# Optimization experiments

Hardware: AMD Instinct MI355X
Metric: run time of the kernel (lower is better)

Reference implementation:

```python
import jax, jax.numpy as jnp
import numpy as np
from jax import lax

NQ = 5  # qubits
NL = 3  # circuit layers


def conv2d(x, w, b):
    y = lax.conv_general_dilated(x, w, (1, 1), 'SAME',
                                 dimension_numbers=('NCHW', 'OIHW', 'NCHW'))
    return y + b[None, :, None, None]


def batchnorm(x, g, b, eps=1e-5):
    # training-mode batch statistics over (N,H,W), matching nn.BatchNorm2d in train()
    mu = x.mean((0, 2, 3), keepdims=True)
    var = x.var((0, 2, 3), keepdims=True)
    return g[None, :, None, None] * (x - mu) * lax.rsqrt(var + eps) + b[None, :, None, None]


def maxpool2(x):
    return lax.reduce_window(x, -jnp.inf, lax.max, (1, 1, 2, 2), (1, 1, 2, 2), 'VALID')


def _apply_1q(state, U, w):
    # state: (2,)*NQ, wire w is axis w (PennyLane default.qubit ordering)
    s = jnp.tensordot(U, state, axes=([1], [w]))
    return jnp.moveaxis(s, 0, w)


def _cnot(state, c, t):
    s0 = jnp.take(state, 0, axis=c)
    s1 = jnp.take(state, 1, axis=c)
    ta = t if t < c else t - 1
    s1 = jnp.flip(s1, axis=ta)  # X on target when control=1
    return jnp.stack([s0, s1], axis=c)


def _rx(t):
    c, s = jnp.cos(t / 2), jnp.sin(t / 2)
    return jnp.array([[c, -1j * s], [-1j * s, c]], dtype=jnp.complex64)


def _ry(t):
    c, s = jnp.cos(t / 2), jnp.sin(t / 2)
    return jnp.array([[c, -s], [s, c]], dtype=jnp.complex64)


def _rz(t):
    e = jnp.exp(-1j * t / 2)
    z = jnp.zeros((), jnp.complex64)
    return jnp.array([[e, z], [z, jnp.conj(e)]], dtype=jnp.complex64)


def quantum_circuit(inputs, weights):
    # inputs: (5,), weights: (30,)  -> scalar <Z0 Z1 Z2>
    state = jnp.zeros((2,) * NQ, jnp.complex64).at[(0,) * NQ].set(1.0)
    npl = NQ * 2  # weights per layer = 10
    nw = weights.shape[0]
    for l in range(NL):
        for i in range(NQ):
            state = _apply_1q(state, _rx(inputs[i]), i)
        for i in range(NQ):
            state = _apply_1q(state, _ry(weights[(l * npl + i) % nw]), i)
            state = _apply_1q(state, _rz(weights[(l * npl + i + NQ) % nw]), i)
        for i in range(NQ - 1):
            state = _cnot(state, i, i + 1)
        state = _cnot(state, NQ - 1, 0)
    probs = jnp.abs(state) ** 2
    z = jnp.array([1.0, -1.0], jnp.float32)
    sign = z[:, None, None] * z[None, :, None] * z[None, None, :]  # Z on wires 0,1,2
    return jnp.sum(probs * sign[:, :, :, None, None])


def setup_inputs() -> dict:
    key = jax.random.key(0)
    ks = jax.random.split(key, 12)
    d = {}
    d['x'] = jax.random.normal(ks[0], (256, 1, 224, 224), jnp.float32)
    d['conv1_w'] = jax.random.normal(ks[1], (16, 1, 3, 3), jnp.float32) * 0.1
    d['conv1_b'] = jnp.zeros((16,), jnp.float32)
    d['bn1_g'] = jnp.ones((16,), jnp.float32)
    d['bn1_b'] = jnp.zeros((16,), jnp.float32)
    d['conv2_w'] = jax.random.normal(ks[2], (32, 16, 3, 3), jnp.float32) * 0.05
    d['conv2_b'] = jnp.zeros((32,), jnp.float32)
    d['bn2_g'] = jnp.ones((32,), jnp.float32)
    d['bn2_b'] = jnp.zeros((32,), jnp.float32)
    d['conv3_w'] = jax.random.normal(ks[3], (64, 32, 3, 3), jnp.float32) * 0.05
    d['conv3_b'] = jnp.zeros((64,), jnp.float32)
    d['bn3_g'] = jnp.ones((64,), jnp.float32)
    d['bn3_b'] = jnp.zeros((64,), jnp.float32)
    d['fc1_w'] = jax.random.normal(ks[4], (64, 5), jnp.float32) * 0.1   # (in,out)
    d['fc1_b'] = jnp.zeros((5,), jnp.float32)
    d['ln_g'] = jnp.ones((5,), jnp.float32)
    d['ln_b'] = jnp.zeros((5,), jnp.float32)
    d['q_params'] = jax.random.uniform(ks[5], (30,), jnp.float32)
    d['fc2_w'] = jax.random.normal(ks[6], (1, 32), jnp.float32) * 0.5
    d['fc2_b'] = jnp.zeros((32,), jnp.float32)
    d['fc3_w'] = jax.random.normal(ks[7], (32, 2), jnp.float32) * 0.2
    d['fc3_b'] = jnp.zeros((2,), jnp.float32)
    return d


def reference(x, conv1_w, conv1_b, bn1_g, bn1_b, conv2_w, conv2_b, bn2_g, bn2_b,
              conv3_w, conv3_b, bn3_g, bn3_b, fc1_w, fc1_b, ln_g, ln_b,
              q_params, fc2_w, fc2_b, fc3_w, fc3_b):
    h = maxpool2(jax.nn.relu(batchnorm(conv2d(x, conv1_w, conv1_b), bn1_g, bn1_b)))
    h = maxpool2(jax.nn.relu(batchnorm(conv2d(h, conv2_w, conv2_b), bn2_g, bn2_b)))
    h = maxpool2(jax.nn.relu(batchnorm(conv2d(h, conv3_w, conv3_b), bn3_g, bn3_b)))
    # dropout is identity in eval; adaptive avg pool (1,1) + flatten
    h = h.mean((2, 3))                    # (B, 64)
    h = h @ fc1_w + fc1_b                 # (B, 5)
    mu = h.mean(-1, keepdims=True)
    var = h.var(-1, keepdims=True)
    h = ln_g * (h - mu) * lax.rsqrt(var + 1e-5) + ln_b
    q = jax.vmap(lambda inp: quantum_circuit(inp, q_params))(h)  # (B,)
    q = q[:, None].astype(jnp.float32)    # (B, 1)
    h2 = jax.nn.relu(q @ fc2_w + fc2_b)   # (B, 32)
    logits = h2 @ fc3_w + fc3_b           # (B, 2)
    return jax.nn.log_softmax(logits, axis=1)
```

## Files before the change

kernel.cpp:

```cpp
#include <hip/hip_runtime.h>
#include <hip/hip_bf16.h>


typedef _Float16 f16;
typedef _Float16 f16x2 __attribute__((ext_vector_type(2)));
typedef _Float16 f16x4 __attribute__((ext_vector_type(4)));
typedef _Float16 f16x8 __attribute__((ext_vector_type(8)));
typedef float f32x4 __attribute__((ext_vector_type(4)));
typedef float f32x16 __attribute__((ext_vector_type(16)));

#define DEV static __device__ __forceinline__

DEV float wave_sum(float v) {
#pragma unroll
  for (int off = 32; off > 0; off >>= 1) v += __shfl_xor(v, off, 64);
  return v;
}

__global__ __launch_bounds__(256) void repack(const float* __restrict__ w2,
                                              const float* __restrict__ w3,
                                              f16* __restrict__ Bt2,
                                              f16* __restrict__ Bt3) {
  int t = blockIdx.x * 256 + threadIdx.x;
  int T = gridDim.x * 256;
  for (int i = t; i < 32 * 168; i += T) {
    int oc = i / 168, kk = i - oc * 168;
    float v = 0.f;
    if (kk < 144) {
      int tap = kk >> 4, ic = kk & 15;
      v = w2[(oc * 16 + ic) * 9 + tap];
    }
    Bt2[i] = (f16)v;
  }
  for (int i = t; i < 64 * 296; i += T) {
    int oc = i / 296, kk = i - oc * 296;
    float v = 0.f;
    if (kk < 288) {
      int tap = kk / 32, ic = kk & 31;
      v = w3[(oc * 32 + ic) * 9 + tap];
    }
    Bt3[i] = (f16)v;
  }
}

__global__ __launch_bounds__(64) void finalize(const float* __restrict__ banks,
                                               const float* __restrict__ g,
                                               const float* __restrict__ b,
                                               float* __restrict__ scsh, int C,
                                               float inv_n) {
  int c = blockIdx.x, bk = threadIdx.x;
  float s = banks[bk * 2 * C + c];
  float qq = banks[bk * 2 * C + C + c];
  s = wave_sum(s);
  qq = wave_sum(qq);
  if (bk == 0) {
    float mean = s * inv_n;
    float var = qq * inv_n - mean * mean;
    float sc = g[c] * rsqrtf(var + 1e-5f);
    scsh[c] = sc;
    scsh[C + c] = b[c] - mean * sc;
  }
}

__global__ __launch_bounds__(256) void l1_mfma32(const float* __restrict__ x,
                                                 const float* __restrict__ w1,
                                                 float* __restrict__ banks,
                                                 f16* __restrict__ h1raw) {
  __shared__ f16 xA[18 * 240];
  __shared__ f16 xB[18 * 240];
  __shared__ f16 lrow[4 * 3616];
  __shared__ float lstat[32];
  int bid = blockIdx.x;
  int n = bid / 14, band = bid - n * 14;
  int y0 = band * 16;
  int t = threadIdx.x;
  if (t < 32) lstat[t] = 0.f;
  for (int i = t; i < 1008; i += 256) {
    int r = i / 56, k = i - r * 56;
    int y = y0 - 1 + r;
    float4 v = make_float4(0.f, 0.f, 0.f, 0.f);
    if ((unsigned)y < 224u)
      v = *(const float4*)(x + ((size_t)(n * 224 + y)) * 224 + k * 4);
    f16 h0 = (f16)v.x, h1 = (f16)v.y, h2 = (f16)v.z, h3 = (f16)v.w;
    f16* pa = xA + r * 240 + 4 * k + 1;
    pa[0] = h0; pa[1] = h1; pa[2] = h2; pa[3] = h3;
    f16x4 pk = {h0, h1, h2, h3};
    *(f16x4*)(xB + r * 240 + 4 * k) = pk;
  }
  if (t < 18) {
    xA[t * 240 + 0] = (f16)0.f;
    xA[t * 240 + 225] = (f16)0.f;
    xA[t * 240 + 226] = (f16)0.f;
    xB[t * 240 + 224] = (f16)0.f;
    xB[t * 240 + 225] = (f16)0.f;
  }
  __syncthreads();

  int wave = t >> 6, lane = t & 63;
  int g = lane >> 5, m32 = lane & 31;
  int oc = m32 & 15, s = m32 >> 4;

  f16x8 b;
#pragma unroll
  for (int j = 0; j < 8; j++) {
    int ky = 2 * g + (j >> 2), kx = j & 3;
    int kys = ky - s;
    float wv = 0.f;
    if (kx < 3 && kys >= 0 && kys < 3) wv = w1[oc * 9 + kys * 3 + kx];
    b[j] = (f16)wv;
  }

  const f16* abase = (m32 & 1) ? (xB + (m32 - 1)) : (xA + m32);
  f16* myrow = lrow + wave * 3616;
  f16* mrow = myrow + s * 1808;
  f32x16 zero16;
#pragma unroll
  for (int r = 0; r < 16; r++) zero16[r] = 0.f;
  const int bp[8] = {0, 1, 4, 5, 8, 9, 12, 13};
  float ssum = 0.f, ssq = 0.f;

  for (int rp = wave; rp < 8; rp += 4) {
    int r0 = 2 * rp + 2 * g;
    const f16* rbase = abase + r0 * 240;
#pragma unroll
    for (int xt = 0; xt < 7; xt++) {
      const f16* p0 = rbase + xt * 32;
      f16x2 v0 = *(const f16x2*)(p0);
      f16x2 v1 = *(const f16x2*)(p0 + 2);
      f16x2 v2 = *(const f16x2*)(p0 + 240);
      f16x2 v3 = *(const f16x2*)(p0 + 242);
      f16x8 a = {v0[0], v0[1], v1[0], v1[1], v2[0], v2[1], v3[0], v3[1]};
      f32x16 acc = __builtin_amdgcn_mfma_f32_32x32x16_f16(a, b, zero16, 0, 0, 0);
#pragma unroll
      for (int r = 0; r < 16; r++) {
        float v = acc[r];
        ssum += v;
        ssq += v * v;
      }
#pragma unroll
      for (int i = 0; i < 8; i++) {
        float pm = fmaxf(acc[2 * i], acc[2 * i + 1]);
        int pxp = xt * 16 + bp[i] + 2 * g;
        mrow[pxp * 16 + oc] = (f16)pm;
      }
    }
    int ph = band * 8 + rp;
    f16* gdst = h1raw + ((size_t)(n * 112) + ph) * 112 * 16;
    for (int i = lane; i < 224; i += 64) {
      f16x8 va = *(const f16x8*)(myrow + i * 8);
      f16x8 vb = *(const f16x8*)(myrow + 1808 + i * 8);
#pragma unroll
      for (int k = 0; k < 8; k++) va[k] = (va[k] > vb[k]) ? va[k] : vb[k];
      *(f16x8*)(gdst + i * 8) = va;
    }
  }
  ssum += __shfl_xor(ssum, 16, 64);
  ssum += __shfl_xor(ssum, 32, 64);
  ssq += __shfl_xor(ssq, 16, 64);
  ssq += __shfl_xor(ssq, 32, 64);
  if (lane < 16) {
    atomicAdd(&lstat[oc], ssum);
    atomicAdd(&lstat[16 + oc], ssq);
  }
  __syncthreads();
  if (t < 32) atomicAdd(&banks[(bid & 63) * 32 + t], lstat[t]);
}

__global__ __launch_bounds__(256, 3) void l2_gemm(
    const f16* __restrict__ h1, const f16* __restrict__ Btg,
    const float* __restrict__ scsh1, f16* __restrict__ p2,
    float* __restrict__ banks) {
  extern __shared__ char smem[];
  f16* lin = (f16*)smem;
  f16* zslot = (f16*)(smem + 32256);
  float* lstat = (float*)(smem + 32288);
  f16* lpool = (f16*)(smem + 32544);
  int bid = blockIdx.x;
  int n = bid / 28, sb = bid - n * 28;
  int t = threadIdx.x;
  int wave = t >> 6, lane = t & 63, q = lane >> 4, wi = lane & 15;
  const int icq = (q & 1) * 8;

  f16x8 breg0[5], breg1[5];
#pragma unroll
  for (int j = 0; j < 5; j++) {
    breg0[j] = *(const f16x8*)(Btg + wi * 168 + j * 32 + q * 8);
    breg1[j] = *(const f16x8*)(Btg + (16 + wi) * 168 + j * 32 + q * 8);
  }

  if (t < 64) lstat[t] = 0.f;
  if (t == 0) {
    f16x8 z = {0, 0, 0, 0, 0, 0, 0, 0};
    *(f16x8*)zslot = z;
  }
#pragma unroll
  for (int k = 0; k < 6; k++) {
    int i = t + k * 256;
    if (i < 1344) {
      int r = i / 224, c = i - r * 224;
      int y = sb * 4 + r - 1;
      f16x8 o = {0, 0, 0, 0, 0, 0, 0, 0};
      if ((unsigned)y < 112u) {
        f16x8 xv =
            *(const f16x8*)(h1 + ((size_t)(n * 112 + y)) * 112 * 16 + c * 8);
        int ch0 = (c & 1) * 8;
#pragma unroll
        for (int e = 0; e < 8; e++) {
          float f = (float)xv[e] * scsh1[ch0 + e] + scsh1[16 + ch0 + e];
          o[e] = (f16)fmaxf(f, 0.f);
        }
      }
      *(f16x8*)(lin + (r * 112 + (c >> 1)) * 24 + (c & 1) * 8) = o;
    }
  }
  __syncthreads();

  f32x4 acc[7][2];
#pragma unroll
  for (int f = 0; f < 7; f++)
#pragma unroll
    for (int nf = 0; nf < 2; nf++)
#pragma unroll
      for (int r = 0; r < 4; r++) acc[f][nf][r] = 0.f;

#pragma unroll
  for (int j = 0; j < 5; j++) {
    const int tA = 2 * j, tB = 2 * j + 1;
    const int kyA = tA / 3, kxA = tA % 3;
    const int kyB = (tB < 9) ? tB / 3 : 0, kxB = (tB < 9) ? tB % 3 : 0;
    bool hiq = (q >= 2);
    int ky = hiq ? kyB : kyA;
    int kx = hiq ? kxB : kxA;
    f16x8 b0 = breg0[j];
    f16x8 b1 = breg1[j];
    int c0 = wi + kx - 1;
    const f16* rowbase = lin + (wave + ky) * 112 * 24 + icq;
#pragma unroll
    for (int f = 0; f < 7; f++) {
      int col = c0 + f * 16;
      const f16* ap =
          ((unsigned)col < 112u) ? (rowbase + col * 24) : (const f16*)zslot;
      f16x8 a = *(const f16x8*)ap;
      acc[f][0] =
          __builtin_amdgcn_mfma_f32_16x16x32_f16(a, b0, acc[f][0], 0, 0, 0);
      acc[f][1] =
          __builtin_amdgcn_mfma_f32_16x16x32_f16(a, b1, acc[f][1], 0, 0, 0);
    }
  }

  float tS0 = 0.f, tQ0 = 0.f, tS1 = 0.f, tQ1 = 0.f;
#pragma unroll
  for (int f = 0; f < 7; f++)
#pragma unroll
    for (int r = 0; r < 4; r++) {
      float v0 = acc[f][0][r], v1 = acc[f][1][r];
      tS0 += v0; tQ0 += v0 * v0;
      tS1 += v1; tQ1 += v1 * v1;
    }
  tS0 += __shfl_xor(tS0, 16, 64); tS0 += __shfl_xor(tS0, 32, 64);
  tQ0 += __shfl_xor(tQ0, 16, 64); tQ0 += __shfl_xor(tQ0, 32, 64);
  tS1 += __shfl_xor(tS1, 16, 64); tS1 += __shfl_xor(tS1, 32, 64);
  tQ1 += __shfl_xor(tQ1, 16, 64); tQ1 += __shfl_xor(tQ1, 32, 64);
  if (q == 0) {
    atomicAdd(&lstat[wi], tS0);
    atomicAdd(&lstat[16 + wi], tS1);
    atomicAdd(&lstat[32 + wi], tQ0);
    atomicAdd(&lstat[48 + wi], tQ1);
  }

  if (wave & 1) {
#pragma unroll
    for (int f = 0; f < 7; f++)
#pragma unroll
      for (int nf = 0; nf < 2; nf++) {
        int ch = nf * 16 + wi;
        int pc0 = f * 8 + q * 2;
        float m0 = fmaxf(acc[f][nf][0], acc[f][nf][1]);
        float m1 = fmaxf(acc[f][nf][2], acc[f][nf][3]);
        lpool[((wave >> 1) * 56 + pc0) * 32 + ch] = (f16)m0;
        lpool[((wave >> 1) * 56 + pc0 + 1) * 32 + ch] = (f16)m1;
      }
  }
  __syncthreads();

  if (!(wave & 1)) {
    int ph = sb * 2 + (wave >> 1);
    size_t ob = (((size_t)n * 56 + ph) * 56) * 32;
#pragma unroll
    for (int f = 0; f < 7; f++)
#pragma unroll
      for (int nf = 0; nf < 2; nf++) {
        int ch = nf * 16 + wi;
        int pc0 = f * 8 + q * 2;
        float m0 = fmaxf(acc[f][nf][0], acc[f][nf][1]);
        float m1 = fmaxf(acc[f][nf][2], acc[f][nf][3]);
        m0 = fmaxf(m0, (float)lpool[((wave >> 1) * 56 + pc0) * 32 + ch]);
        m1 = fmaxf(m1, (float)lpool[((wave >> 1) * 56 + pc0 + 1) * 32 + ch]);
        p2[ob + (size_t)pc0 * 32 + ch] = (f16)m0;
        p2[ob + (size_t)(pc0 + 1) * 32 + ch] = (f16)m1;
      }
  }

  if (t < 64) {
    int i = t >> 5, c = t & 31;
    atomicAdd(&banks[(bid & 63) * 64 + i * 32 + c], lstat[i * 32 + c]);
  }
}

__global__ __launch_bounds__(256, 2) void l3_gemm(
    const f16* __restrict__ p2, const f16* __restrict__ Btg,
    const float* __restrict__ scsh2, f16* __restrict__ p3,
    float* __restrict__ banks) {
  extern __shared__ char smem[];
  f16* lin = (f16*)smem;
  float* lstat = (float*)(smem + 46400);
  f16* lpool = (f16*)smem;
  int bx = blockIdx.x;
  int n = bx / 7, sb = bx - n * 7;
  int t = threadIdx.x;
  int wave = t >> 6, lane = t & 63, q = lane >> 4, wi = lane & 15;

  f16x8 breg[9][4];
#pragma unroll
  for (int j = 0; j < 9; j++)
#pragma unroll
    for (int h = 0; h < 4; h++)
      breg[j][h] =
          *(const f16x8*)(Btg + (h * 16 + wi) * 296 + j * 32 + q * 8);

  if (t < 128) lstat[t] = 0.f;
#pragma unroll
  for (int k = 0; k < 9; k++) {
    int i = t + k * 256;
    if (i < 2240) {
      int r = i / 224, rem = i - r * 224;
      int c = rem >> 2, cp = rem & 3;
      int y = sb * 8 + r - 1;
      f16x8 o = {0, 0, 0, 0, 0, 0, 0, 0};
      if ((unsigned)y < 56u) {
        f16x8 xv =
            *(const f16x8*)(p2 + (((size_t)(n * 56 + y)) * 56 + c) * 32 +
                            cp * 8);
        int ch0 = cp * 8;
#pragma unroll
        for (int e = 0; e < 8; e++) {
          float f = (float)xv[e] * scsh2[ch0 + e] + scsh2[32 + ch0 + e];
          o[e] = (f16)fmaxf(f, 0.f);
        }
      }
      *(f16x8*)(lin + (r * 58 + 1 + c) * 40 + cp * 8) = o;
    }
  }
  if (t < 80) {
    int r = t / 8, k = t & 7;
    int col = (k < 4) ? 0 : 57, cp = k & 3;
    f16x8 z = {0, 0, 0, 0, 0, 0, 0, 0};
    *(f16x8*)(lin + (r * 58 + col) * 40 + cp * 8) = z;
  }
  __syncthreads();

  int abase[7];
#pragma unroll
  for (int f = 0; f < 7; f++) {
    int pos = wave * 112 + f * 16 + wi;
    int r = pos / 56, w = pos - r * 56;
    abase[f] = (r * 58 + w) * 40 + q * 8;
  }
  f32x4 acc[7][4];
#pragma unroll
  for (int f = 0; f < 7; f++)
#pragma unroll
    for (int h = 0; h < 4; h++)
#pragma unroll
      for (int r = 0; r < 4; r++) acc[f][h][r] = 0.f;

#pragma unroll
  for (int j = 0; j < 9; j++) {
    const int ky = j / 3, kx = j % 3;
#pragma unroll
    for (int f = 0; f < 7; f++) {
      f16x8 a = *(const f16x8*)(lin + abase[f] + (ky * 58 + kx) * 40);
#pragma unroll
      for (int h = 0; h < 4; h++)
        acc[f][h] =
            __builtin_amdgcn_mfma_f32_16x16x32_f16(a, breg[j][h], acc[f][h],
                                                   0, 0, 0);
    }
  }

  float tS[4] = {0.f, 0.f, 0.f, 0.f}, tQ[4] = {0.f, 0.f, 0.f, 0.f};
#pragma unroll
  for (int f = 0; f < 7; f++)
#pragma unroll
    for (int h = 0; h < 4; h++)
#pragma unroll
      for (int r = 0; r < 4; r++) {
        float v = acc[f][h][r];
        tS[h] += v;
        tQ[h] += v * v;
      }
#pragma unroll
  for (int h = 0; h < 4; h++) {
    tS[h] += __shfl_xor(tS[h], 16, 64); tS[h] += __shfl_xor(tS[h], 32, 64);
    tQ[h] += __shfl_xor(tQ[h], 16, 64); tQ[h] += __shfl_xor(tQ[h], 32, 64);
  }
  if (q == 0) {
#pragma unroll
    for (int h = 0; h < 4; h++) {
      atomicAdd(&lstat[h * 16 + wi], tS[h]);
      atomicAdd(&lstat[64 + h * 16 + wi], tQ[h]);
    }
  }
  __syncthreads();

#pragma unroll
  for (int f = 0; f < 7; f++) {
    int pos = wave * 112 + f * 16 + q * 4;
    int r0 = pos / 56, w0 = pos - r0 * 56;
#pragma unroll
    for (int h = 0; h < 4; h++) {
      int ch = h * 16 + wi;
      float m0 = fmaxf(acc[f][h][0], acc[f][h][1]);
      float m1 = fmaxf(acc[f][h][2], acc[f][h][3]);
      lpool[(r0 * 28 + (w0 >> 1)) * 64 + ch] = (f16)m0;
      lpool[(r0 * 28 + (w0 >> 1) + 1) * 64 + ch] = (f16)m1;
    }
  }
  __syncthreads();

  for (int i = t; i < 7168; i += 256) {
    int ch = i & 63, rest = i >> 6;
    int pc = rest % 28, pr = rest / 28;
    float v = fmaxf((float)lpool[((2 * pr) * 28 + pc) * 64 + ch],
                    (float)lpool[((2 * pr + 1) * 28 + pc) * 64 + ch]);
    int gpr = sb * 4 + pr;
    p3[(((size_t)n * 28 + gpr) * 28 + pc) * 64 + ch] = (f16)v;
  }
  if (t < 128) {
    atomicAdd(&banks[(bx & 63) * 128 + t], lstat[t]);
  }
}

__global__ __launch_bounds__(256) void head_pool(
    const f16* __restrict__ p3, const float* __restrict__ scsh3,
    const float* __restrict__ fc1w, const float* __restrict__ fc1b,
    float* __restrict__ featg) {
  int n = blockIdx.x, t = threadIdx.x;
  __shared__ float red[64 * 33];
  __shared__ float meanc[64];
  int oct = t & 7, strip = t >> 3;
  float sc[8], sh[8];
#pragma unroll
  for (int k = 0; k < 8; k++) {
    sc[k] = scsh3[oct * 8 + k];
    sh[k] = scsh3[64 + oct * 8 + k];
  }
  float acc[8];
#pragma unroll
  for (int k = 0; k < 8; k++) acc[k] = 0.f;
  const f16* base = p3 + (size_t)n * 50176 + oct * 8;
  for (int px = strip; px < 784; px += 32) {
    f16x8 v = *(const f16x8*)(base + (size_t)px * 64);
#pragma unroll
    for (int k = 0; k < 8; k++)
      acc[k] += fmaxf((float)v[k] * sc[k] + sh[k], 0.f);
  }
#pragma unroll
  for (int k = 0; k < 8; k++) red[(oct * 8 + k) * 33 + strip] = acc[k];
  __syncthreads();
  if (t < 64) {
    float s = 0.f;
    for (int j = 0; j < 32; j++) s += red[t * 33 + j];
    meanc[t] = s * (1.f / 784.f);
  }
  __syncthreads();
  if (t < 5) {
    float a = fc1b[t];
    for (int i = 0; i < 64; i++) a += meanc[i] * fc1w[i * 5 + t];
    featg[n * 8 + t] = a;
  }
}

template <int W>
DEV void g_rx(float (&sr)[32], float (&si)[32], float c, float s) {
  constexpr int m = 1 << (4 - W);
#pragma unroll
  for (int i0 = 0; i0 < 32; i0++)
    if (!(i0 & m)) {
      int i1 = i0 | m;
      float a0r = sr[i0], a0i = si[i0], a1r = sr[i1], a1i = si[i1];
      sr[i0] = c * a0r + s * a1i;
      si[i0] = c * a0i - s * a1r;
      sr[i1] = s * a0i + c * a1r;
      si[i1] = -s * a0r + c * a1i;
    }
}

template <int W>
DEV void g_ry(float (&sr)[32], float (&si)[32], float c, float s) {
  constexpr int m = 1 << (4 - W);
#pragma unroll
  for (int i0 = 0; i0 < 32; i0++)
    if (!(i0 & m)) {
      int i1 = i0 | m;
      float a0r = sr[i0], a0i = si[i0], a1r = sr[i1], a1i = si[i1];
      sr[i0] = c * a0r - s * a1r;
      si[i0] = c * a0i - s * a1i;
      sr[i1] = s * a0r + c * a1r;
      si[i1] = s * a0i + c * a1i;
    }
}

template <int W>
DEV void g_rz(float (&sr)[32], float (&si)[32], float c, float s) {
  constexpr int m = 1 << (4 - W);
#pragma unroll
  for (int i0 = 0; i0 < 32; i0++)
    if (!(i0 & m)) {
      int i1 = i0 | m;
      float a0r = sr[i0], a0i = si[i0], a1r = sr[i1], a1i = si[i1];
      sr[i0] = c * a0r + s * a0i;
      si[i0] = c * a0i - s * a0r;
      sr[i1] = c * a1r - s * a1i;
      si[i1] = c * a1i + s * a1r;
    }
}

template <int C, int T>
DEV void g_cnot(float (&sr)[32], float (&si)[32]) {
  constexpr int mc = 1 << (4 - C), mt = 1 << (4 - T);
#pragma unroll
  for (int i0 = 0; i0 < 32; i0++)
    if ((i0 & mc) && !(i0 & mt)) {
      int i1 = i0 | mt;
      float tr = sr[i0]; sr[i0] = sr[i1]; sr[i1] = tr;
      float ti = si[i0]; si[i0] = si[i1]; si[i1] = ti;
    }
}

__global__ __launch_bounds__(64) void head_q(
    const float* __restrict__ featg, const float* __restrict__ lng,
    const float* __restrict__ lnb, const float* __restrict__ qp,
    const float* __restrict__ fc2w, const float* __restrict__ fc2b,
    const float* __restrict__ fc3w, const float* __restrict__ fc3b,
    float* __restrict__ out) {
  int n = blockIdx.x * 64 + threadIdx.x;
  float f[5];
#pragma unroll
  for (int i = 0; i < 5; i++) f[i] = featg[n * 8 + i];
  float mu = (f[0] + f[1] + f[2] + f[3] + f[4]) * 0.2f;
  float var = 0.f;
#pragma unroll
  for (int i = 0; i < 5; i++) { float d = f[i] - mu; var += d * d; }
  var *= 0.2f;
  float inv = rsqrtf(var + 1e-5f);
#pragma unroll
  for (int i = 0; i < 5; i++) f[i] = lng[i] * (f[i] - mu) * inv + lnb[i];

  float cx[5], sx[5];
#pragma unroll
  for (int i = 0; i < 5; i++) {
    cx[i] = cosf(0.5f * f[i]);
    sx[i] = sinf(0.5f * f[i]);
  }
  float sr[32], si[32];
#pragma unroll
  for (int i = 0; i < 32; i++) { sr[i] = 0.f; si[i] = 0.f; }
  sr[0] = 1.f;

  for (int l = 0; l < 3; l++) {
    g_rx<0>(sr, si, cx[0], sx[0]);
    g_rx<1>(sr, si, cx[1], sx[1]);
    g_rx<2>(sr, si, cx[2], sx[2]);
    g_rx<3>(sr, si, cx[3], sx[3]);
    g_rx<4>(sr, si, cx[4], sx[4]);
#define WIRE_YZ(I)                                             \
  {                                                            \
    float ty = qp[l * 10 + I];                                 \
    g_ry<I>(sr, si, cosf(0.5f * ty), sinf(0.5f * ty));         \
    float tz = qp[l * 10 + I + 5];                             \
    g_rz<I>(sr, si, cosf(0.5f * tz), sinf(0.5f * tz));         \
  }
    WIRE_YZ(0) WIRE_YZ(1) WIRE_YZ(2) WIRE_YZ(3) WIRE_YZ(4)
#undef WIRE_YZ
    g_cnot<0, 1>(sr, si);
    g_cnot<1, 2>(sr, si);
    g_cnot<2, 3>(sr, si);
    g_cnot<3, 4>(sr, si);
    g_cnot<4, 0>(sr, si);
  }
  float qv = 0.f;
#pragma unroll
  for (int idx = 0; idx < 32; idx++) {
    float p = sr[idx] * sr[idx] + si[idx] * si[idx];
    qv += (__popc(idx & 0x1C) & 1) ? -p : p;
  }
  float l0 = fc3b[0], l1 = fc3b[1];
  for (int j = 0; j < 32; j++) {
    float hv = fmaxf(qv * fc2w[j] + fc2b[j], 0.f);
    l0 += hv * fc3w[j * 2];
    l1 += hv * fc3w[j * 2 + 1];
  }
  float mx = fmaxf(l0, l1);
  float lse = mx + logf(expf(l0 - mx) + expf(l1 - mx));
  out[n * 2 + 0] = l0 - lse;
  out[n * 2 + 1] = l1 - lse;
}

extern "C" void kernel_launch(void* const* d_in, const int* in_sizes, int n_in,
                              void* d_out, int out_size, void* d_ws,
                              size_t ws_size, hipStream_t stream) {
  const float* x    = (const float*)d_in[0];
  const float* w1   = (const float*)d_in[1];
  const float* bn1g = (const float*)d_in[3];
  const float* bn1b = (const float*)d_in[4];
  const float* w2   = (const float*)d_in[5];
  const float* bn2g = (const float*)d_in[7];
  const float* bn2b = (const float*)d_in[8];
  const float* w3   = (const float*)d_in[9];
  const float* bn3g = (const float*)d_in[11];
  const float* bn3b = (const float*)d_in[12];
  const float* fc1w = (const float*)d_in[13];
  const float* fc1b = (const float*)d_in[14];
  const float* lng  = (const float*)d_in[15];
  const float* lnb  = (const float*)d_in[16];
  const float* qp   = (const float*)d_in[17];
  const float* fc2w = (const float*)d_in[18];
  const float* fc2b = (const float*)d_in[19];
  const float* fc3w = (const float*)d_in[20];
  const float* fc3b = (const float*)d_in[21];
  float* out = (float*)d_out;

  char* ws = (char*)d_ws;
  float* banks1 = (float*)ws;
  float* banks2 = (float*)(ws + 8192);
  float* banks3 = (float*)(ws + 24576);
  float* scsh1 = (float*)(ws + 57344);
  float* scsh2 = (float*)(ws + 57472);
  float* scsh3 = (float*)(ws + 57728);
  f16* Bt2 = (f16*)(ws + 58240);
  f16* Bt3 = (f16*)(ws + 68992);
  f16* h1 = (f16*)(ws + 106880);
  f16* p2 = (f16*)(ws + 106880 + 102760448ULL);
  f16* p3 = (f16*)(ws + 106880 + 102760448ULL + 51380224ULL);
  float* featg = banks2;

  hipMemsetAsync(ws, 0, 57344, stream);
  repack<<<16, 256, 0, stream>>>(w2, w3, Bt2, Bt3);
  l1_mfma32<<<3584, 256, 0, stream>>>(x, w1, banks1, h1);
  finalize<<<16, 64, 0, stream>>>(banks1, bn1g, bn1b, scsh1, 16,
                                  1.f / 12845056.f);
  l2_gemm<<<7168, 256, 39712, stream>>>(h1, Bt2, scsh1, p2, banks2);
  finalize<<<32, 64, 0, stream>>>(banks2, bn2g, bn2b, scsh2, 32,
                                  1.f / 3211264.f);
  l3_gemm<<<1792, 256, 46912, stream>>>(p2, Bt3, scsh2, p3, banks3);
  finalize<<<64, 64, 0, stream>>>(banks3, bn3g, bn3b, scsh3, 64,
                                  1.f / 802816.f);
  head_pool<<<256, 256, 0, stream>>>(p3, scsh3, fc1w, fc1b, featg);
  head_q<<<4, 64, 0, stream>>>(featg, lng, lnb, qp, fc2w, fc2b, fc3w, fc3b,
                               out);
}
```

Before: 343.4 us.

## Fold weight repack, BN3 finalize and quantum head into neighboring kernels

The weight repack moves into the first 16 blocks of the layer-1 kernel. The BN3 statistics reduction is recomputed per block inside head_pool. The quantum circuit head now runs in the last-arriving head_pool block, found through an atomic counter and a threadfence. This removes three kernel launches and the gaps between them. In exchange, 16 layer-1 blocks carry extra work, every head_pool block redundantly reduces the banks, and the quantum head runs on a single block of 256 threads instead of 4 blocks of 64.

```diff
diff --git a/kernel.cpp b/kernel.cpp
--- a/kernel.cpp
+++ b/kernel.cpp
@@ -15,32 +15,6 @@
 #pragma unroll
   for (int off = 32; off > 0; off >>= 1) v += __shfl_xor(v, off, 64);
   return v;
-}
-
-__global__ __launch_bounds__(256) void repack(const float* __restrict__ w2,
-                                              const float* __restrict__ w3,
-                                              f16* __restrict__ Bt2,
-                                              f16* __restrict__ Bt3) {
-  int t = blockIdx.x * 256 + threadIdx.x;
-  int T = gridDim.x * 256;
-  for (int i = t; i < 32 * 168; i += T) {
-    int oc = i / 168, kk = i - oc * 168;
-    float v = 0.f;
-    if (kk < 144) {
-      int tap = kk >> 4, ic = kk & 15;
-      v = w2[(oc * 16 + ic) * 9 + tap];
-    }
-    Bt2[i] = (f16)v;
-  }
-  for (int i = t; i < 64 * 296; i += T) {
-    int oc = i / 296, kk = i - oc * 296;
-    float v = 0.f;
-    if (kk < 288) {
-      int tap = kk / 32, ic = kk & 31;
-      v = w3[(oc * 32 + ic) * 9 + tap];
-    }
-    Bt3[i] = (f16)v;
-  }
 }
 
 __global__ __launch_bounds__(64) void finalize(const float* __restrict__ banks,
@@ -62,18 +36,43 @@
   }
 }
 
-__global__ __launch_bounds__(256) void l1_mfma32(const float* __restrict__ x,
-                                                 const float* __restrict__ w1,
-                                                 float* __restrict__ banks,
-                                                 f16* __restrict__ h1raw) {
+__global__ __launch_bounds__(256) void l1_mfma32(
+    const float* __restrict__ x, const float* __restrict__ w1,
+    float* __restrict__ banks, f16* __restrict__ h1raw,
+    const float* __restrict__ w2, const float* __restrict__ w3,
+    f16* __restrict__ Bt2, f16* __restrict__ Bt3) {
   __shared__ f16 xA[18 * 240];
   __shared__ f16 xB[18 * 240];
   __shared__ f16 lrow[4 * 3616];
   __shared__ float lstat[32];
   int bid = blockIdx.x;
+  int t = threadIdx.x;
+
+  if (bid < 16) {
+    int tt = bid * 256 + t;
+    const int T = 4096;
+    for (int i = tt; i < 32 * 168; i += T) {
+      int oc = i / 168, kk = i - oc * 168;
+      float v = 0.f;
+      if (kk < 144) {
+        int tap = kk >> 4, ic = kk & 15;
+        v = w2[(oc * 16 + ic) * 9 + tap];
+      }
+      Bt2[i] = (f16)v;
+    }
+    for (int i = tt; i < 64 * 296; i += T) {
+      int oc = i / 296, kk = i - oc * 296;
+      float v = 0.f;
+      if (kk < 288) {
+        int tap = kk / 32, ic = kk & 31;
+        v = w3[(oc * 32 + ic) * 9 + tap];
+      }
+      Bt3[i] = (f16)v;
+    }
+  }
+
   int n = bid / 14, band = bid - n * 14;
   int y0 = band * 16;
-  int t = threadIdx.x;
   if (t < 32) lstat[t] = 0.f;
   for (int i = t; i < 1008; i += 256) {
     int r = i / 56, k = i - r * 56;
@@ -441,46 +440,6 @@
   }
 }
 
-__global__ __launch_bounds__(256) void head_pool(
-    const f16* __restrict__ p3, const float* __restrict__ scsh3,
-    const float* __restrict__ fc1w, const float* __restrict__ fc1b,
-    float* __restrict__ featg) {
-  int n = blockIdx.x, t = threadIdx.x;
-  __shared__ float red[64 * 33];
-  __shared__ float meanc[64];
-  int oct = t & 7, strip = t >> 3;
-  float sc[8], sh[8];
-#pragma unroll
-  for (int k = 0; k < 8; k++) {
-    sc[k] = scsh3[oct * 8 + k];
-    sh[k] = scsh3[64 + oct * 8 + k];
-  }
-  float acc[8];
-#pragma unroll
-  for (int k = 0; k < 8; k++) acc[k] = 0.f;
-  const f16* base = p3 + (size_t)n * 50176 + oct * 8;
-  for (int px = strip; px < 784; px += 32) {
-    f16x8 v = *(const f16x8*)(base + (size_t)px * 64);
-#pragma unroll
-    for (int k = 0; k < 8; k++)
-      acc[k] += fmaxf((float)v[k] * sc[k] + sh[k], 0.f);
-  }
-#pragma unroll
-  for (int k = 0; k < 8; k++) red[(oct * 8 + k) * 33 + strip] = acc[k];
-  __syncthreads();
-  if (t < 64) {
-    float s = 0.f;
-    for (int j = 0; j < 32; j++) s += red[t * 33 + j];
-    meanc[t] = s * (1.f / 784.f);
-  }
-  __syncthreads();
-  if (t < 5) {
-    float a = fc1b[t];
-    for (int i = 0; i < 64; i++) a += meanc[i] * fc1w[i * 5 + t];
-    featg[n * 8 + t] = a;
-  }
-}
-
 template <int W>
 DEV void g_rx(float (&sr)[32], float (&si)[32], float c, float s) {
   constexpr int m = 1 << (4 - W);
@@ -538,73 +497,150 @@
     }
 }
 
-__global__ __launch_bounds__(64) void head_q(
-    const float* __restrict__ featg, const float* __restrict__ lng,
-    const float* __restrict__ lnb, const float* __restrict__ qp,
-    const float* __restrict__ fc2w, const float* __restrict__ fc2b,
-    const float* __restrict__ fc3w, const float* __restrict__ fc3b,
-    float* __restrict__ out) {
-  int n = blockIdx.x * 64 + threadIdx.x;
-  float f[5];
-#pragma unroll
-  for (int i = 0; i < 5; i++) f[i] = featg[n * 8 + i];
-  float mu = (f[0] + f[1] + f[2] + f[3] + f[4]) * 0.2f;
-  float var = 0.f;
-#pragma unroll
-  for (int i = 0; i < 5; i++) { float d = f[i] - mu; var += d * d; }
-  var *= 0.2f;
-  float inv = rsqrtf(var + 1e-5f);
-#pragma unroll
-  for (int i = 0; i < 5; i++) f[i] = lng[i] * (f[i] - mu) * inv + lnb[i];
-
-  float cx[5], sx[5];
-#pragma unroll
-  for (int i = 0; i < 5; i++) {
-    cx[i] = cosf(0.5f * f[i]);
-    sx[i] = sinf(0.5f * f[i]);
-  }
-  float sr[32], si[32];
-#pragma unroll
-  for (int i = 0; i < 32; i++) { sr[i] = 0.f; si[i] = 0.f; }
-  sr[0] = 1.f;
-
-  for (int l = 0; l < 3; l++) {
-    g_rx<0>(sr, si, cx[0], sx[0]);
-    g_rx<1>(sr, si, cx[1], sx[1]);
-    g_rx<2>(sr, si, cx[2], sx[2]);
-    g_rx<3>(sr, si, cx[3], sx[3]);
-    g_rx<4>(sr, si, cx[4], sx[4]);
-#define WIRE_YZ(I)                                             \
-  {                                                            \
-    float ty = qp[l * 10 + I];                                 \
-    g_ry<I>(sr, si, cosf(0.5f * ty), sinf(0.5f * ty));         \
-    float tz = qp[l * 10 + I + 5];                             \
-    g_rz<I>(sr, si, cosf(0.5f * tz), sinf(0.5f * tz));         \
-  }
-    WIRE_YZ(0) WIRE_YZ(1) WIRE_YZ(2) WIRE_YZ(3) WIRE_YZ(4)
+__global__ __launch_bounds__(256) void head_pool(
+    const f16* __restrict__ p3, const float* __restrict__ banks3,
+    const float* __restrict__ bn3g, const float* __restrict__ bn3b,
+    const float* __restrict__ fc1w, const float* __restrict__ fc1b,
+    const float* __restrict__ lng, const float* __restrict__ lnb,
+    const float* __restrict__ qp, const float* __restrict__ fc2w,
+    const float* __restrict__ fc2b, const float* __restrict__ fc3w,
+    const float* __restrict__ fc3b, float* __restrict__ featg,
+    unsigned int* __restrict__ counter, float* __restrict__ out) {
+  __shared__ float red[64 * 33];
+  __shared__ float meanc[64];
+  __shared__ float scshL[128];
+  __shared__ float part[2][4][64];
+  __shared__ int lastFlag;
+  int n = blockIdx.x, t = threadIdx.x;
+
+  {
+    int c = t & 63, grp = t >> 6;
+    float s = 0.f, qq = 0.f;
+#pragma unroll
+    for (int i = 0; i < 16; i++) {
+      int bk = grp * 16 + i;
+      s += banks3[bk * 128 + c];
+      qq += banks3[bk * 128 + 64 + c];
+    }
+    part[0][grp][c] = s;
+    part[1][grp][c] = qq;
+  }
+  __syncthreads();
+  if (t < 64) {
+    float s = part[0][0][t] + part[0][1][t] + part[0][2][t] + part[0][3][t];
+    float qq = part[1][0][t] + part[1][1][t] + part[1][2][t] + part[1][3][t];
+    float mean = s * (1.f / 802816.f);
+    float var = qq * (1.f / 802816.f) - mean * mean;
+    float sc = bn3g[t] * rsqrtf(var + 1e-5f);
+    scshL[t] = sc;
+    scshL[64 + t] = bn3b[t] - mean * sc;
+  }
+  __syncthreads();
+
+  int oct = t & 7, strip = t >> 3;
+  float sc[8], sh[8];
+#pragma unroll
+  for (int k = 0; k < 8; k++) {
+    sc[k] = scshL[oct * 8 + k];
+    sh[k] = scshL[64 + oct * 8 + k];
+  }
+  float acc[8];
+#pragma unroll
+  for (int k = 0; k < 8; k++) acc[k] = 0.f;
+  const f16* base = p3 + (size_t)n * 50176 + oct * 8;
+  for (int px = strip; px < 784; px += 32) {
+    f16x8 v = *(const f16x8*)(base + (size_t)px * 64);
+#pragma unroll
+    for (int k = 0; k < 8; k++)
+      acc[k] += fmaxf((float)v[k] * sc[k] + sh[k], 0.f);
+  }
+#pragma unroll
+  for (int k = 0; k < 8; k++) red[(oct * 8 + k) * 33 + strip] = acc[k];
+  __syncthreads();
+  if (t < 64) {
+    float s = 0.f;
+    for (int j = 0; j < 32; j++) s += red[t * 33 + j];
+    meanc[t] = s * (1.f / 784.f);
+  }
+  __syncthreads();
+  if (t < 5) {
+    float a = fc1b[t];
+    for (int i = 0; i < 64; i++) a += meanc[i] * fc1w[i * 5 + t];
+    featg[n * 8 + t] = a;
+  }
+
+  __threadfence();
+  __syncthreads();
+  if (t == 0) {
+    unsigned int done = atomicAdd(counter, 1u);
+    lastFlag = (done == gridDim.x - 1) ? 1 : 0;
+  }
+  __syncthreads();
+  if (!lastFlag) return;
+
+  {
+    int nn = t;
+    float f[5];
+#pragma unroll
+    for (int i = 0; i < 5; i++) f[i] = featg[nn * 8 + i];
+    float mu = (f[0] + f[1] + f[2] + f[3] + f[4]) * 0.2f;
+    float var = 0.f;
+#pragma unroll
+    for (int i = 0; i < 5; i++) { float d = f[i] - mu; var += d * d; }
+    var *= 0.2f;
+    float inv = rsqrtf(var + 1e-5f);
+#pragma unroll
+    for (int i = 0; i < 5; i++) f[i] = lng[i] * (f[i] - mu) * inv + lnb[i];
+
+    float cx[5], sx[5];
+#pragma unroll
+    for (int i = 0; i < 5; i++) {
+      cx[i] = cosf(0.5f * f[i]);
+      sx[i] = sinf(0.5f * f[i]);
+    }
+    float sr[32], si[32];
+#pragma unroll
+    for (int i = 0; i < 32; i++) { sr[i] = 0.f; si[i] = 0.f; }
+    sr[0] = 1.f;
+
+    for (int l = 0; l < 3; l++) {
+      g_rx<0>(sr, si, cx[0], sx[0]);
+      g_rx<1>(sr, si, cx[1], sx[1]);
+      g_rx<2>(sr, si, cx[2], sx[2]);
+      g_rx<3>(sr, si, cx[3], sx[3]);
+      g_rx<4>(sr, si, cx[4], sx[4]);
+#define WIRE_YZ(I)                                           \
+  {                                                          \
+    float ty = qp[l * 10 + I];                               \
+    g_ry<I>(sr, si, cosf(0.5f * ty), sinf(0.5f * ty));       \
+    float tz = qp[l * 10 + I + 5];                           \
+    g_rz<I>(sr, si, cosf(0.5f * tz), sinf(0.5f * tz));       \
+  }
+      WIRE_YZ(0) WIRE_YZ(1) WIRE_YZ(2) WIRE_YZ(3) WIRE_YZ(4)
 #undef WIRE_YZ
-    g_cnot<0, 1>(sr, si);
-    g_cnot<1, 2>(sr, si);
-    g_cnot<2, 3>(sr, si);
-    g_cnot<3, 4>(sr, si);
-    g_cnot<4, 0>(sr, si);
-  }
-  float qv = 0.f;
-#pragma unroll
-  for (int idx = 0; idx < 32; idx++) {
-    float p = sr[idx] * sr[idx] + si[idx] * si[idx];
-    qv += (__popc(idx & 0x1C) & 1) ? -p : p;
-  }
-  float l0 = fc3b[0], l1 = fc3b[1];
-  for (int j = 0; j < 32; j++) {
-    float hv = fmaxf(qv * fc2w[j] + fc2b[j], 0.f);
-    l0 += hv * fc3w[j * 2];
-    l1 += hv * fc3w[j * 2 + 1];
-  }
-  float mx = fmaxf(l0, l1);
-  float lse = mx + logf(expf(l0 - mx) + expf(l1 - mx));
-  out[n * 2 + 0] = l0 - lse;
-  out[n * 2 + 1] = l1 - lse;
+      g_cnot<0, 1>(sr, si);
+      g_cnot<1, 2>(sr, si);
+      g_cnot<2, 3>(sr, si);
+      g_cnot<3, 4>(sr, si);
+      g_cnot<4, 0>(sr, si);
+    }
+    float qv = 0.f;
+#pragma unroll
+    for (int idx = 0; idx < 32; idx++) {
+      float p = sr[idx] * sr[idx] + si[idx] * si[idx];
+      qv += (__popc(idx & 0x1C) & 1) ? -p : p;
+    }
+    float l0 = fc3b[0], l1 = fc3b[1];
+    for (int j = 0; j < 32; j++) {
+      float hv = fmaxf(qv * fc2w[j] + fc2b[j], 0.f);
+      l0 += hv * fc3w[j * 2];
+      l1 += hv * fc3w[j * 2 + 1];
+    }
+    float mx = fmaxf(l0, l1);
+    float lse = mx + logf(expf(l0 - mx) + expf(l1 - mx));
+    out[nn * 2 + 0] = l0 - lse;
+    out[nn * 2 + 1] = l1 - lse;
+  }
 }
 
 extern "C" void kernel_launch(void* const* d_in, const int* in_sizes, int n_in,
@@ -638,25 +674,24 @@
   float* scsh1 = (float*)(ws + 57344);
   float* scsh2 = (float*)(ws + 57472);
   float* scsh3 = (float*)(ws + 57728);
-  f16* Bt2 = (f16*)(ws + 58240);
-  f16* Bt3 = (f16*)(ws + 68992);
-  f16* h1 = (f16*)(ws + 106880);
-  f16* p2 = (f16*)(ws + 106880 + 102760448ULL);
-  f16* p3 = (f16*)(ws + 106880 + 102760448ULL + 51380224ULL);
+  unsigned int* counter = (unsigned int*)(ws + 58240);
+  f16* Bt2 = (f16*)(ws + 58304);
+  f16* Bt3 = (f16*)(ws + 69056);
+  f16* h1 = (f16*)(ws + 106944);
+  f16* p2 = (f16*)(ws + 106944 + 102760448ULL);
+  f16* p3 = (f16*)(ws + 106944 + 102760448ULL + 51380224ULL);
   float* featg = banks2;
-
-  hipMemsetAsync(ws, 0, 57344, stream);
-  repack<<<16, 256, 0, stream>>>(w2, w3, Bt2, Bt3);
-  l1_mfma32<<<3584, 256, 0, stream>>>(x, w1, banks1, h1);
+  (void)scsh3;
+
+  hipMemsetAsync(ws, 0, 58304, stream);
+  l1_mfma32<<<3584, 256, 0, stream>>>(x, w1, banks1, h1, w2, w3, Bt2, Bt3);
   finalize<<<16, 64, 0, stream>>>(banks1, bn1g, bn1b, scsh1, 16,
                                   1.f / 12845056.f);
   l2_gemm<<<7168, 256, 39712, stream>>>(h1, Bt2, scsh1, p2, banks2);
   finalize<<<32, 64, 0, stream>>>(banks2, bn2g, bn2b, scsh2, 32,
                                   1.f / 3211264.f);
   l3_gemm<<<1792, 256, 46912, stream>>>(p2, Bt3, scsh2, p3, banks3);
-  finalize<<<64, 64, 0, stream>>>(banks3, bn3g, bn3b, scsh3, 64,
-                                  1.f / 802816.f);
-  head_pool<<<256, 256, 0, stream>>>(p3, scsh3, fc1w, fc1b, featg);
-  head_q<<<4, 64, 0, stream>>>(featg, lng, lnb, qp, fc2w, fc2b, fc3w, fc3b,
-                               out);
-}
+  head_pool<<<256, 256, 0, stream>>>(p3, banks3, bn3g, bn3b, fc1w, fc1b,
+                                     lng, lnb, qp, fc2w, fc2b, fc3w, fc3b,
+                                     featg, counter, out);
+}
```

Measured after the change: 354.1 us. +3.1%, slower.
